# Kernel tuning notes

Hardware: AMD Instinct MI355X
Metric: run time of the kernel (lower is better)

Reference implementation:

```python
import jax, jax.numpy as jnp
import numpy as np

CODEBOOK = 512
EMB_DIM = 64
COMMITMENT_COST = 0.25


def setup_inputs() -> dict:
    key = jax.random.key(0)
    k1, k2 = jax.random.split(key)
    inputs = jax.random.normal(k1, (32, EMB_DIM, 64, 64), dtype=jnp.float32)
    # nn.Embedding weight initialized uniform(-1/code_book_dim, 1/code_book_dim)
    embedding = jax.random.uniform(
        k2, (CODEBOOK, EMB_DIM), dtype=jnp.float32,
        minval=-1.0 / CODEBOOK, maxval=1.0 / CODEBOOK)
    return {"inputs": inputs, "embedding": embedding}


def reference(inputs, embedding):
    B, C, H, W = inputs.shape          # C == embedding_dim
    D = embedding.shape[1]
    x = jnp.transpose(inputs, (0, 2, 3, 1))      # [B,H,W,D] (permute(0,2,3,1))
    flat = x.reshape(-1, D)                       # [N,D]
    x2 = jnp.sum(flat * flat, axis=1, keepdims=True)          # [N,1]
    e2 = jnp.sum(embedding * embedding, axis=1)[None, :]       # [1,K]
    xe = flat @ embedding.T                                    # [N,K]
    distances = (x2 - 2.0 * xe + e2) / D                       # [N,K]
    encoding_indices = jnp.argmin(distances, axis=1)           # [N]
    quantized = embedding[encoding_indices].reshape(x.shape)   # [B,H,W,D]
    # MSE losses with detach semantics
    e_latent_loss = jnp.mean((jax.lax.stop_gradient(quantized) - x) ** 2)
    q_latent_loss = jnp.mean((quantized - jax.lax.stop_gradient(x)) ** 2)
    loss = q_latent_loss + COMMITMENT_COST * e_latent_loss
    # straight-through estimator (module default training=True)
    quantized_st = x + jax.lax.stop_gradient(quantized - x)
    out = jnp.transpose(quantized_st, (0, 3, 1, 2))            # back to NCHW
    indices = encoding_indices.reshape(B, -1)                  # [B, H*W]
    return loss, out, indices
```

## Files before the change

### kernel.cpp

```cpp
#include <hip/hip_runtime.h>


#define KCODE 512
#define EMB   64
#define HWSZ  4096
#define NPOS  131072
#define DELTA 2.5e-4f

typedef short short8  __attribute__((ext_vector_type(8)));
typedef float float4v __attribute__((ext_vector_type(4)));


__device__ __forceinline__ float np_sumsq64(const float* a) {
    #pragma clang fp contract(off)
    {
        float r0 = a[0] * a[0], r1 = a[1] * a[1], r2 = a[2] * a[2], r3 = a[3] * a[3];
        float r4 = a[4] * a[4], r5 = a[5] * a[5], r6 = a[6] * a[6], r7 = a[7] * a[7];
        for (int i = 8; i < 64; i += 8) {
            r0 += a[i + 0] * a[i + 0];
            r1 += a[i + 1] * a[i + 1];
            r2 += a[i + 2] * a[i + 2];
            r3 += a[i + 3] * a[i + 3];
            r4 += a[i + 4] * a[i + 4];
            r5 += a[i + 5] * a[i + 5];
            r6 += a[i + 6] * a[i + 6];
            r7 += a[i + 7] * a[i + 7];
        }
        return ((r0 + r1) + (r2 + r3)) + ((r4 + r5) + (r6 + r7));
    }
}

__device__ __forceinline__ float exact_u(const float* x, float x2,
                                         const float* ek, float e2k) {
    float t0 = 0.f, t1 = 0.f, t2 = 0.f, t3 = 0.f;
    #pragma unroll
    for (int c = 0; c < EMB; c += 4) {
        t0 = fmaf(x[c + 0], ek[c + 0], t0);
        t1 = fmaf(x[c + 1], ek[c + 1], t1);
        t2 = fmaf(x[c + 2], ek[c + 2], t2);
        t3 = fmaf(x[c + 3], ek[c + 3], t3);
    }
    float xe  = (t0 + t1) + (t2 + t3);
    float tmp = x2 - 2.0f * xe;
    return tmp + e2k;
}

__device__ __forceinline__ unsigned short bf16rne(float f) {
    unsigned u = __float_as_uint(f);
    unsigned r = (u + 0x7FFFu + ((u >> 16) & 1u)) >> 16;
    return (unsigned short)r;
}
__device__ __forceinline__ float bf16tof(unsigned short h) {
    return __uint_as_float((unsigned)h << 16);
}

#define INS(M1, I1, M2, I2, M3, v, i)                      \
    {                                                      \
        bool lt1 = (v) < (M1), lt2 = (v) < (M2), lt3 = (v) < (M3); \
        (M3) = lt2 ? (M2) : (lt3 ? (v) : (M3));            \
        (I2) = lt1 ? (I1) : (lt2 ? (i) : (I2));            \
        (M2) = lt1 ? (M1) : (lt2 ? (v) : (M2));            \
        (M1) = lt1 ? (v) : (M1);                           \
        (I1) = lt1 ? (i) : (I1);                           \
    }

__global__ void vq_prep(const float* __restrict__ emb, float* __restrict__ ws) {
    int f = blockIdx.x * blockDim.x + threadIdx.x;
    if (f == 0) { ((unsigned*)ws)[0] = 0u; ((unsigned*)ws)[1] = 0u; }
    if (f < KCODE) ws[520 + f] = np_sumsq64(emb + f * EMB);
    short8* bfrag = (short8*)(ws + 1032);
    int l = f & 63;
    int c = (f >> 6) & 1;
    int t = f >> 7;
    int code  = t * 16 + (l & 15);
    int dbase = 32 * c + ((l >> 4) & 3) * 8;
    const float* e = emb + code * EMB + dbase;
    short8 h, lo;
    #pragma unroll
    for (int j = 0; j < 8; ++j) {
        float v = e[j];
        unsigned short hb = bf16rne(v);
        float hf = bf16tof(hb);
        unsigned short lb = bf16rne(v - hf);
        h[j]  = (short)hb;
        lo[j] = (short)lb;
    }
    bfrag[t * 256 + c * 128 + 0 * 64 + l] = h;
    bfrag[t * 256 + c * 128 + 1 * 64 + l] = lo;
}

__global__ __launch_bounds__(256, 3) void vq_screen(
        const float*  __restrict__ in,
        const float*  __restrict__ e2np,
        const short8* __restrict__ bfrag,
        float*        __restrict__ out_idx,
        unsigned*     __restrict__ fullCnt,
        unsigned*     __restrict__ fullList,
        int fullCap) {
    const int tid  = threadIdx.x;
    const int wave = tid >> 6;
    const int lane = tid & 63;
    const int lg   = lane >> 4;
    const int lc   = lane & 15;
    const int wavePos = blockIdx.x * 128 + wave * 32;

    short8 fH[2][2], fL[2][2];
    #pragma unroll
    for (int pt = 0; pt < 2; ++pt) {
        int pos = wavePos + pt * 16 + lc;
        int b   = pos >> 12;
        int hw  = pos & (HWSZ - 1);
        const float* xb = in + ((size_t)b << 18) + hw;
        #pragma unroll
        for (int c = 0; c < 2; ++c) {
            short8 h, lo;
            #pragma unroll
            for (int j = 0; j < 8; ++j) {
                int d = 32 * c + lg * 8 + j;
                float g = -2.0f * xb[(size_t)d << 12];
                unsigned short hb = bf16rne(g);
                float hf = bf16tof(hb);
                unsigned short lb = bf16rne(g - hf);
                h[j]  = (short)hb;
                lo[j] = (short)lb;
            }
            fH[pt][c] = h;
            fL[pt][c] = lo;
        }
    }

    float m1[2][4], m2[2][4], m3[2][4];
    int   i1[2][4], i2[2][4];
    #pragma unroll
    for (int pt = 0; pt < 2; ++pt)
        #pragma unroll
        for (int r = 0; r < 4; ++r) {
            m1[pt][r] = 3.4e38f; m2[pt][r] = 3.4e38f; m3[pt][r] = 3.4e38f;
            i1[pt][r] = 0;       i2[pt][r] = 0;
        }

    short8 ceh0 = bfrag[lane],       cel0 = bfrag[64 + lane];
    short8 ceh1 = bfrag[128 + lane], cel1 = bfrag[192 + lane];
    float  ce2  = e2np[lc];
    #pragma unroll 2
    for (int t = 0; t < 32; ++t) {
        short8 neh0, nel0, neh1, nel1;
        float  ne2 = 0.0f;
        if (t < 31) {
            const short8* nb = bfrag + (t + 1) * 256;
            neh0 = nb[lane];       nel0 = nb[64 + lane];
            neh1 = nb[128 + lane]; nel1 = nb[192 + lane];
            ne2  = e2np[(t + 1) * 16 + lc];
        }
        const int kf = t * 16 + lc;
        #pragma unroll
        for (int pt = 0; pt < 2; ++pt) {
            float4v aH = {ce2, ce2, ce2, ce2};
            float4v aM = {0.f, 0.f, 0.f, 0.f};
            float4v aL = {0.f, 0.f, 0.f, 0.f};
            aH = __builtin_amdgcn_mfma_f32_16x16x32_bf16(fH[pt][0], ceh0, aH, 0, 0, 0);
            aM = __builtin_amdgcn_mfma_f32_16x16x32_bf16(fH[pt][0], cel0, aM, 0, 0, 0);
            aL = __builtin_amdgcn_mfma_f32_16x16x32_bf16(fL[pt][0], ceh0, aL, 0, 0, 0);
            aH = __builtin_amdgcn_mfma_f32_16x16x32_bf16(fH[pt][1], ceh1, aH, 0, 0, 0);
            aM = __builtin_amdgcn_mfma_f32_16x16x32_bf16(fH[pt][1], cel1, aM, 0, 0, 0);
            aL = __builtin_amdgcn_mfma_f32_16x16x32_bf16(fL[pt][1], ceh1, aL, 0, 0, 0);
            #pragma unroll
            for (int r = 0; r < 4; ++r) {
                float sv = (aH[r] + aM[r]) + aL[r];
                INS(m1[pt][r], i1[pt][r], m2[pt][r], i2[pt][r], m3[pt][r], sv, kf);
            }
        }
        ceh0 = neh0; cel0 = nel0; ceh1 = neh1; cel1 = nel1; ce2 = ne2;
    }

    #pragma unroll
    for (int pt = 0; pt < 2; ++pt) {
        #pragma unroll
        for (int r = 0; r < 4; ++r) {
            float M1 = m1[pt][r], M2 = m2[pt][r], M3 = m3[pt][r];
            int   I1 = i1[pt][r], I2 = i2[pt][r];
            #pragma unroll
            for (int d = 1; d <= 8; d <<= 1) {
                float pm1 = __shfl_xor(M1, d, 64);
                int   pi1 = __shfl_xor(I1, d, 64);
                float pm2 = __shfl_xor(M2, d, 64);
                int   pi2 = __shfl_xor(I2, d, 64);
                float pm3 = __shfl_xor(M3, d, 64);
                INS(M1, I1, M2, I2, M3, pm1, pi1);
                INS(M1, I1, M2, I2, M3, pm2, pi2);
                M3 = fminf(M3, pm3);
            }
            m1[pt][r] = M1; m2[pt][r] = M2; m3[pt][r] = M3;
            i1[pt][r] = I1; i2[pt][r] = I2;
        }
    }

    if (lc == 0) {
        #pragma unroll
        for (int pt = 0; pt < 2; ++pt) {
            #pragma unroll
            for (int r = 0; r < 4; ++r) {
                int p  = wavePos + pt * 16 + lg * 4 + r;
                int g2 = (m2[pt][r] - m1[pt][r] <= DELTA) ? 1 : 0;
                int g3 = (m3[pt][r] - m1[pt][r] <= DELTA) ? 1 : 0;
                int packed = i1[pt][r] | (i2[pt][r] << 9) | (g2 << 18) | (g3 << 19);
                out_idx[p] = (float)packed;
                if (g3) {
                    unsigned slot = atomicAdd(fullCnt, 1u);
                    if (slot < (unsigned)fullCap) fullList[slot] = (unsigned)p;
                }
            }
        }
    }
}

__global__ __launch_bounds__(64) void vq_full(
        const float* __restrict__ in, const float* __restrict__ emb,
        const float* __restrict__ e2np, const unsigned* __restrict__ fullCnt,
        const unsigned* __restrict__ fullList, int fullCap,
        float* __restrict__ out_idx) {
    __shared__ float xs[64];
    const int lane = threadIdx.x;
    unsigned cnt = *fullCnt;
    if (cnt > (unsigned)fullCap) cnt = (unsigned)fullCap;
    for (unsigned idx = blockIdx.x; idx < cnt; idx += gridDim.x) {
        int n = (int)fullList[idx];
        int b = n >> 12, hw = n & (HWSZ - 1);
        __syncthreads();
        xs[lane] = in[((size_t)b << 18) + ((size_t)lane << 12) + hw];
        __syncthreads();
        float x2 = np_sumsq64(xs);
        float bu = 3.4e38f;
        int   bk = 0x7fffffff;
        for (int j = 0; j < 8; ++j) {
            int k = j * 64 + lane;
            float u = exact_u(xs, x2, emb + k * EMB, e2np[k]);
            if (u < bu || (u == bu && k < bk)) { bu = u; bk = k; }
        }
        #pragma unroll
        for (int d = 1; d < 64; d <<= 1) {
            float ou = __shfl_xor(bu, d, 64);
            int   ok = __shfl_xor(bk, d, 64);
            if (ou < bu || (ou == bu && ok < bk)) { bu = ou; bk = ok; }
        }
        if (lane == 0) out_idx[n] = (float)bk;
    }
}

__global__ __launch_bounds__(256) void vq_write(
        const float* __restrict__ in, const float* __restrict__ emb,
        const float* __restrict__ e2np,
        float* __restrict__ out_idx, float* __restrict__ out_q,
        float* __restrict__ partials,
        unsigned* __restrict__ ticket,
        float* __restrict__ out_loss) {
    const int tid = threadIdx.x;
    const int n   = blockIdx.x * 256 + tid;
    const int b   = n >> 12;
    const int hw  = n & (HWSZ - 1);

    const float* xp = in + ((size_t)b << 18) + hw;
    float x[EMB];
    #pragma unroll
    for (int c = 0; c < EMB; ++c) x[c] = xp[(size_t)c << 12];

    int v = (int)out_idx[n];
    int k = v & 511;
    int fl = v >> 18;
    if (fl) {
        float x2 = np_sumsq64(x);
        if (fl & 2) {
            float bu = 3.4e38f; int bk = 0;
            for (int kk = 0; kk < KCODE; ++kk) {
                float u = exact_u(x, x2, emb + kk * EMB, e2np[kk]);
                if (u < bu) { bu = u; bk = kk; }
            }
            k = bk;
        } else {
            int ia = v & 511, ib = (v >> 9) & 511;
            float u1 = exact_u(x, x2, emb + ia * EMB, e2np[ia]);
            float u2 = exact_u(x, x2, emb + ib * EMB, e2np[ib]);
            k = (u1 < u2) ? ia : (u2 < u1 ? ib : (ia < ib ? ia : ib));
        }
    }
    out_idx[n] = (float)k;

    const float4* qk = (const float4*)(emb + (size_t)k * EMB);
    float* op = out_q + ((size_t)b << 18) + hw;
    float s = 0.0f;
    #pragma unroll
    for (int c4 = 0; c4 < EMB / 4; ++c4) {
        float4 q = qk[c4];
        float d0 = q.x - x[c4 * 4 + 0];
        float d1 = q.y - x[c4 * 4 + 1];
        float d2 = q.z - x[c4 * 4 + 2];
        float d3 = q.w - x[c4 * 4 + 3];
        s = fmaf(d0, d0, s); s = fmaf(d1, d1, s);
        s = fmaf(d2, d2, s); s = fmaf(d3, d3, s);
        op[(size_t)(c4 * 4 + 0) << 12] = q.x;
        op[(size_t)(c4 * 4 + 1) << 12] = q.y;
        op[(size_t)(c4 * 4 + 2) << 12] = q.z;
        op[(size_t)(c4 * 4 + 3) << 12] = q.w;
    }

    #pragma unroll
    for (int off = 32; off > 0; off >>= 1)
        s += __shfl_down(s, off, 64);
    __shared__ float red[4];
    const int wave = tid >> 6;
    const int lane = tid & 63;
    if (lane == 0) red[wave] = s;
    __syncthreads();
    if (tid == 0) {
        partials[blockIdx.x] = (red[0] + red[1]) + (red[2] + red[3]);
        __threadfence();
        unsigned tk = atomicAdd(ticket, 1u);
        if (tk == 511u) {
            __threadfence();
            float a0 = 0.f, a1 = 0.f, a2 = 0.f, a3 = 0.f;
            float a4 = 0.f, a5 = 0.f, a6 = 0.f, a7 = 0.f;
            for (int i = 0; i < 512; i += 8) {
                a0 += partials[i + 0]; a1 += partials[i + 1];
                a2 += partials[i + 2]; a3 += partials[i + 3];
                a4 += partials[i + 4]; a5 += partials[i + 5];
                a6 += partials[i + 6]; a7 += partials[i + 7];
            }
            float tot = ((a0 + a1) + (a2 + a3)) + ((a4 + a5) + (a6 + a7));
            out_loss[0] = 1.25f * tot * (1.0f / ((float)NPOS * (float)EMB));
        }
    }
}

extern "C" void kernel_launch(void* const* d_in, const int* in_sizes, int n_in,
                              void* d_out, int out_size, void* d_ws, size_t ws_size,
                              hipStream_t stream) {
    const float* in  = (const float*)d_in[0];
    const float* emb = (const float*)d_in[1];
    float* ws  = (float*)d_ws;
    float* out = (float*)d_out;

    float*    out_loss = out;
    float*    out_q    = out + 1;
    float*    out_idx  = out + 1 + (size_t)NPOS * EMB;
    unsigned* fullCnt  = (unsigned*)ws;
    unsigned* ticket   = (unsigned*)ws + 1;
    float*    partials = ws + 8;
    float*    e2np     = ws + 520;
    short8*   bfrag    = (short8*)(ws + 1032);
    unsigned* fullList = (unsigned*)(ws + 33800);

    long avail = (long)(ws_size / 4) - 33800;
    int  fullCap = avail > 0 ? (avail > 1024 ? 1024 : (int)avail) : 0;

    vq_prep<<<16, 256, 0, stream>>>(emb, ws);
    vq_screen<<<NPOS / 128, 256, 0, stream>>>(in, e2np, bfrag, out_idx,
                                              fullCnt, fullList, fullCap);
    vq_full<<<256, 64, 0, stream>>>(in, emb, e2np, fullCnt, fullList, fullCap,
                                    out_idx);
    vq_write<<<NPOS / 256, 256, 0, stream>>>(in, emb, e2np, out_idx, out_q,
                                             partials, ticket, out_loss);
}
```

Before: 203.4 us.

## Drop full-search kernel; split write kernel across two threads per position with wave-cooperative fallback

Removes the separate vq_full kernel and its atomic work list. Ambiguous positions are now handled inside vq_write by a wave-cooperative search, where lanes share x through shuffles and each lane scans 8 codes. vq_write now uses two threads per position, each handling 32 channels, which halves per-thread registers and doubles the thread count to raise occupancy. The costs are a ballot loop that serialises rare full searches within a wave, plus extra loads of the other half of x for two-candidate refinement.

Result: slower. 279.3 us (+37.3%).

```diff
diff --git a/kernel.cpp b/kernel.cpp
--- a/kernel.cpp
+++ b/kernel.cpp
@@ -30,15 +30,75 @@
     }
 }
 
-__device__ __forceinline__ float exact_u(const float* x, float x2,
-                                         const float* ek, float e2k) {
+__device__ __forceinline__ float np_sumsq64_split(const float* a, const float* o) {
+    #pragma clang fp contract(off)
+    {
+        float r0 = a[0] * a[0], r1 = a[1] * a[1], r2 = a[2] * a[2], r3 = a[3] * a[3];
+        float r4 = a[4] * a[4], r5 = a[5] * a[5], r6 = a[6] * a[6], r7 = a[7] * a[7];
+        for (int i = 8; i < 32; i += 8) {
+            r0 += a[i + 0] * a[i + 0];  r1 += a[i + 1] * a[i + 1];
+            r2 += a[i + 2] * a[i + 2];  r3 += a[i + 3] * a[i + 3];
+            r4 += a[i + 4] * a[i + 4];  r5 += a[i + 5] * a[i + 5];
+            r6 += a[i + 6] * a[i + 6];  r7 += a[i + 7] * a[i + 7];
+        }
+        for (int i = 0; i < 32; i += 8) {
+            r0 += o[i + 0] * o[i + 0];  r1 += o[i + 1] * o[i + 1];
+            r2 += o[i + 2] * o[i + 2];  r3 += o[i + 3] * o[i + 3];
+            r4 += o[i + 4] * o[i + 4];  r5 += o[i + 5] * o[i + 5];
+            r6 += o[i + 6] * o[i + 6];  r7 += o[i + 7] * o[i + 7];
+        }
+        return ((r0 + r1) + (r2 + r3)) + ((r4 + r5) + (r6 + r7));
+    }
+}
+
+__device__ __forceinline__ float exact_u_split2(const float* a, const float* o,
+                                                float x2, const float* ek,
+                                                float e2k) {
     float t0 = 0.f, t1 = 0.f, t2 = 0.f, t3 = 0.f;
     #pragma unroll
-    for (int c = 0; c < EMB; c += 4) {
-        t0 = fmaf(x[c + 0], ek[c + 0], t0);
-        t1 = fmaf(x[c + 1], ek[c + 1], t1);
-        t2 = fmaf(x[c + 2], ek[c + 2], t2);
-        t3 = fmaf(x[c + 3], ek[c + 3], t3);
+    for (int c = 0; c < 32; c += 4) {
+        t0 = fmaf(a[c + 0], ek[c + 0], t0);
+        t1 = fmaf(a[c + 1], ek[c + 1], t1);
+        t2 = fmaf(a[c + 2], ek[c + 2], t2);
+        t3 = fmaf(a[c + 3], ek[c + 3], t3);
+    }
+    #pragma unroll
+    for (int c = 0; c < 32; c += 4) {
+        t0 = fmaf(o[c + 0], ek[32 + c + 0], t0);
+        t1 = fmaf(o[c + 1], ek[32 + c + 1], t1);
+        t2 = fmaf(o[c + 2], ek[32 + c + 2], t2);
+        t3 = fmaf(o[c + 3], ek[32 + c + 3], t3);
+    }
+    float xe  = (t0 + t1) + (t2 + t3);
+    float tmp = x2 - 2.0f * xe;
+    return tmp + e2k;
+}
+
+__device__ __forceinline__ float np_sumsq64_shfl(float xl) {
+    #pragma clang fp contract(off)
+    {
+        float r[8];
+        #pragma unroll
+        for (int j = 0; j < 8; ++j) { float v = __shfl(xl, j, 64); r[j] = v * v; }
+        #pragma unroll
+        for (int i = 8; i < 64; i += 8)
+            #pragma unroll
+            for (int j = 0; j < 8; ++j) {
+                float v = __shfl(xl, i + j, 64);
+                r[j] += v * v;
+            }
+        return ((r[0] + r[1]) + (r[2] + r[3])) + ((r[4] + r[5]) + (r[6] + r[7]));
+    }
+}
+__device__ __forceinline__ float exact_u_shfl(float xl, float x2,
+                                              const float* ek, float e2k) {
+    float t0 = 0.f, t1 = 0.f, t2 = 0.f, t3 = 0.f;
+    #pragma unroll
+    for (int c = 0; c < 64; c += 4) {
+        t0 = fmaf(__shfl(xl, c + 0, 64), ek[c + 0], t0);
+        t1 = fmaf(__shfl(xl, c + 1, 64), ek[c + 1], t1);
+        t2 = fmaf(__shfl(xl, c + 2, 64), ek[c + 2], t2);
+        t3 = fmaf(__shfl(xl, c + 3, 64), ek[c + 3], t3);
     }
     float xe  = (t0 + t1) + (t2 + t3);
     float tmp = x2 - 2.0f * xe;
@@ -67,8 +127,8 @@
 __global__ void vq_prep(const float* __restrict__ emb, float* __restrict__ ws) {
     int f = blockIdx.x * blockDim.x + threadIdx.x;
     if (f == 0) { ((unsigned*)ws)[0] = 0u; ((unsigned*)ws)[1] = 0u; }
-    if (f < KCODE) ws[520 + f] = np_sumsq64(emb + f * EMB);
-    short8* bfrag = (short8*)(ws + 1032);
+    if (f < KCODE) ws[1032 + f] = np_sumsq64(emb + f * EMB);
+    short8* bfrag = (short8*)(ws + 1544);
     int l = f & 63;
     int c = (f >> 6) & 1;
     int t = f >> 7;
@@ -93,10 +153,7 @@
         const float*  __restrict__ in,
         const float*  __restrict__ e2np,
         const short8* __restrict__ bfrag,
-        float*        __restrict__ out_idx,
-        unsigned*     __restrict__ fullCnt,
-        unsigned*     __restrict__ fullList,
-        int fullCap) {
+        float*        __restrict__ out_idx) {
     const int tid  = threadIdx.x;
     const int wave = tid >> 6;
     const int lane = tid & 63;
@@ -205,45 +262,8 @@
                 int g3 = (m3[pt][r] - m1[pt][r] <= DELTA) ? 1 : 0;
                 int packed = i1[pt][r] | (i2[pt][r] << 9) | (g2 << 18) | (g3 << 19);
                 out_idx[p] = (float)packed;
-                if (g3) {
-                    unsigned slot = atomicAdd(fullCnt, 1u);
-                    if (slot < (unsigned)fullCap) fullList[slot] = (unsigned)p;
-                }
-            }
-        }
-    }
-}
-
-__global__ __launch_bounds__(64) void vq_full(
-        const float* __restrict__ in, const float* __restrict__ emb,
-        const float* __restrict__ e2np, const unsigned* __restrict__ fullCnt,
-        const unsigned* __restrict__ fullList, int fullCap,
-        float* __restrict__ out_idx) {
-    __shared__ float xs[64];
-    const int lane = threadIdx.x;
-    unsigned cnt = *fullCnt;
-    if (cnt > (unsigned)fullCap) cnt = (unsigned)fullCap;
-    for (unsigned idx = blockIdx.x; idx < cnt; idx += gridDim.x) {
-        int n = (int)fullList[idx];
-        int b = n >> 12, hw = n & (HWSZ - 1);
-        __syncthreads();
-        xs[lane] = in[((size_t)b << 18) + ((size_t)lane << 12) + hw];
-        __syncthreads();
-        float x2 = np_sumsq64(xs);
-        float bu = 3.4e38f;
-        int   bk = 0x7fffffff;
-        for (int j = 0; j < 8; ++j) {
-            int k = j * 64 + lane;
-            float u = exact_u(xs, x2, emb + k * EMB, e2np[k]);
-            if (u < bu || (u == bu && k < bk)) { bu = u; bk = k; }
-        }
-        #pragma unroll
-        for (int d = 1; d < 64; d <<= 1) {
-            float ou = __shfl_xor(bu, d, 64);
-            int   ok = __shfl_xor(bk, d, 64);
-            if (ou < bu || (ou == bu && ok < bk)) { bu = ou; bk = ok; }
-        }
-        if (lane == 0) out_idx[n] = (float)bk;
+            }
+        }
     }
 }
 
@@ -254,47 +274,75 @@
         float* __restrict__ partials,
         unsigned* __restrict__ ticket,
         float* __restrict__ out_loss) {
-    const int tid = threadIdx.x;
-    const int n   = blockIdx.x * 256 + tid;
-    const int b   = n >> 12;
-    const int hw  = n & (HWSZ - 1);
-
-    const float* xp = in + ((size_t)b << 18) + hw;
-    float x[EMB];
-    #pragma unroll
-    for (int c = 0; c < EMB; ++c) x[c] = xp[(size_t)c << 12];
-
-    int v = (int)out_idx[n];
-    int k = v & 511;
-    int fl = v >> 18;
-    if (fl) {
-        float x2 = np_sumsq64(x);
-        if (fl & 2) {
-            float bu = 3.4e38f; int bk = 0;
-            for (int kk = 0; kk < KCODE; ++kk) {
-                float u = exact_u(x, x2, emb + kk * EMB, e2np[kk]);
-                if (u < bu) { bu = u; bk = kk; }
-            }
-            k = bk;
-        } else {
-            int ia = v & 511, ib = (v >> 9) & 511;
-            float u1 = exact_u(x, x2, emb + ia * EMB, e2np[ia]);
-            float u2 = exact_u(x, x2, emb + ib * EMB, e2np[ib]);
-            k = (u1 < u2) ? ia : (u2 < u1 ? ib : (ia < ib ? ia : ib));
-        }
-    }
-    out_idx[n] = (float)k;
-
-    const float4* qk = (const float4*)(emb + (size_t)k * EMB);
-    float* op = out_q + ((size_t)b << 18) + hw;
+    const int tid  = threadIdx.x;
+    const int wave = tid >> 6;
+    const int lane = tid & 63;
+    const int g    = blockIdx.x * 256 + tid;
+    const int p    = g >> 1;
+    const int h    = g & 1;
+    const int b    = p >> 12;
+    const int hw   = p & (HWSZ - 1);
+
+    const float* xp = in + ((size_t)b << 18) + ((size_t)(h * 32) << 12) + hw;
+    float xh[32];
+    #pragma unroll
+    for (int c = 0; c < 32; ++c) xh[c] = xp[(size_t)c << 12];
+
+    int v  = (int)out_idx[p];
+    int kk = v & 511;
+    const int fl = v >> 18;
+
+    if (fl == 1 && h == 0) {
+        float xo[32];
+        const float* xp2 = in + ((size_t)b << 18) + ((size_t)32 << 12) + hw;
+        #pragma unroll
+        for (int c = 0; c < 32; ++c) xo[c] = xp2[(size_t)c << 12];
+        float x2 = np_sumsq64_split(xh, xo);
+        int ia = v & 511, ib = (v >> 9) & 511;
+        float u1 = exact_u_split2(xh, xo, x2, emb + ia * EMB, e2np[ia]);
+        float u2 = exact_u_split2(xh, xo, x2, emb + ib * EMB, e2np[ib]);
+        kk = (u1 < u2) ? ia : (u2 < u1 ? ib : (ia < ib ? ia : ib));
+    }
+
+    unsigned long long bm = __ballot((fl & 2) != 0 && h == 0);
+    while (bm) {
+        const int src = __ffsll((long long)bm) - 1;
+        bm &= bm - 1;
+        const int pn  = (blockIdx.x * 256 + wave * 64 + src) >> 1;
+        const int bb  = pn >> 12;
+        const int hww = pn & (HWSZ - 1);
+        float xl = in[((size_t)bb << 18) + ((size_t)lane << 12) + hww];
+        float x2 = np_sumsq64_shfl(xl);
+        float bu = 3.4e38f;
+        int   bk = 0x7fffffff;
+        #pragma unroll
+        for (int j = 0; j < 8; ++j) {
+            int k = j * 64 + lane;
+            float u = exact_u_shfl(xl, x2, emb + (size_t)k * EMB, e2np[k]);
+            if (u < bu || (u == bu && k < bk)) { bu = u; bk = k; }
+        }
+        #pragma unroll
+        for (int d = 1; d < 64; d <<= 1) {
+            float ou = __shfl_xor(bu, d, 64);
+            int   ok = __shfl_xor(bk, d, 64);
+            if (ou < bu || (ou == bu && ok < bk)) { bu = ou; bk = ok; }
+        }
+        if ((lane >> 1) == (src >> 1)) kk = bk;
+    }
+
+    kk = __shfl(kk, lane & ~1, 64);
+    if (h == 0) out_idx[p] = (float)kk;
+
+    const float4* q4 = (const float4*)(emb + (size_t)kk * EMB + h * 32);
+    float* op = out_q + ((size_t)b << 18) + ((size_t)(h * 32) << 12) + hw;
     float s = 0.0f;
     #pragma unroll
-    for (int c4 = 0; c4 < EMB / 4; ++c4) {
-        float4 q = qk[c4];
-        float d0 = q.x - x[c4 * 4 + 0];
-        float d1 = q.y - x[c4 * 4 + 1];
-        float d2 = q.z - x[c4 * 4 + 2];
-        float d3 = q.w - x[c4 * 4 + 3];
+    for (int c4 = 0; c4 < 8; ++c4) {
+        float4 q = q4[c4];
+        float d0 = q.x - xh[c4 * 4 + 0];
+        float d1 = q.y - xh[c4 * 4 + 1];
+        float d2 = q.z - xh[c4 * 4 + 2];
+        float d3 = q.w - xh[c4 * 4 + 3];
         s = fmaf(d0, d0, s); s = fmaf(d1, d1, s);
         s = fmaf(d2, d2, s); s = fmaf(d3, d3, s);
         op[(size_t)(c4 * 4 + 0) << 12] = q.x;
@@ -307,19 +355,17 @@
     for (int off = 32; off > 0; off >>= 1)
         s += __shfl_down(s, off, 64);
     __shared__ float red[4];
-    const int wave = tid >> 6;
-    const int lane = tid & 63;
     if (lane == 0) red[wave] = s;
     __syncthreads();
     if (tid == 0) {
         partials[blockIdx.x] = (red[0] + red[1]) + (red[2] + red[3]);
         __threadfence();
         unsigned tk = atomicAdd(ticket, 1u);
-        if (tk == 511u) {
+        if (tk == 1023u) {
             __threadfence();
             float a0 = 0.f, a1 = 0.f, a2 = 0.f, a3 = 0.f;
             float a4 = 0.f, a5 = 0.f, a6 = 0.f, a7 = 0.f;
-            for (int i = 0; i < 512; i += 8) {
+            for (int i = 0; i < 1024; i += 8) {
                 a0 += partials[i + 0]; a1 += partials[i + 1];
                 a2 += partials[i + 2]; a3 += partials[i + 3];
                 a4 += partials[i + 4]; a5 += partials[i + 5];
@@ -342,21 +388,13 @@
     float*    out_loss = out;
     float*    out_q    = out + 1;
     float*    out_idx  = out + 1 + (size_t)NPOS * EMB;
-    unsigned* fullCnt  = (unsigned*)ws;
     unsigned* ticket   = (unsigned*)ws + 1;
     float*    partials = ws + 8;
-    float*    e2np     = ws + 520;
-    short8*   bfrag    = (short8*)(ws + 1032);
-    unsigned* fullList = (unsigned*)(ws + 33800);
-
-    long avail = (long)(ws_size / 4) - 33800;
-    int  fullCap = avail > 0 ? (avail > 1024 ? 1024 : (int)avail) : 0;
+    float*    e2np     = ws + 1032;
+    short8*   bfrag    = (short8*)(ws + 1544);
 
     vq_prep<<<16, 256, 0, stream>>>(emb, ws);
-    vq_screen<<<NPOS / 128, 256, 0, stream>>>(in, e2np, bfrag, out_idx,
-                                              fullCnt, fullList, fullCap);
-    vq_full<<<256, 64, 0, stream>>>(in, emb, e2np, fullCnt, fullList, fullCap,
-                                    out_idx);
-    vq_write<<<NPOS / 256, 256, 0, stream>>>(in, emb, e2np, out_idx, out_q,
-                                             partials, ticket, out_loss);
-}
+    vq_screen<<<NPOS / 128, 256, 0, stream>>>(in, e2np, bfrag, out_idx);
+    vq_write<<<NPOS * 2 / 256, 256, 0, stream>>>(in, emb, e2np, out_idx, out_q,
+                                                 partials, ticket, out_loss);
+}
```
